# Optimization experiments

Measured on AMD Instinct MI355X. Metric: run time of the kernel, lower is better.

Reference implementation:

```python
import jax, jax.numpy as jnp
import numpy as np

B, S = 4, 4096
D_MODEL = 1024
INDEXER_DIM = 64
LOCAL_WINDOW = 16
MEDIUM_WINDOW = 64
GLOBAL_K = 32
LOCAL_SPARSE = 0.8


def _local_k_schedule(seq_len):
    # Replicates torch: k_local = max(1, int(L * (1 - local_sparse))) with Python float math
    ks = []
    for q in range(seq_len):
        L = min(q + 1, LOCAL_WINDOW)
        ks.append(max(1, int(L * (1.0 - LOCAL_SPARSE))))
    ks = np.asarray(ks, dtype=np.int32)
    return ks, int(ks.max())


def setup_inputs() -> dict:
    key = jax.random.key(0)
    kx, kl, km, kg = jax.random.split(key, 4)
    scale = D_MODEL ** -0.5
    return {
        "x": jax.random.normal(kx, (B, S, D_MODEL), jnp.float32),
        "W_local": jax.random.normal(kl, (INDEXER_DIM, D_MODEL), jnp.float32) * scale,
        "W_medium": jax.random.normal(km, (INDEXER_DIM, D_MODEL), jnp.float32) * scale,
        "W_global": jax.random.normal(kg, (INDEXER_DIM, D_MODEL), jnp.float32) * scale,
    }


def reference(x, W_local, W_medium, W_global):
    Bb, Ss, _ = x.shape
    neg_inf = jnp.array(-jnp.inf, x.dtype)
    zero = jnp.array(0.0, x.dtype)

    lf = x @ W_local.T   # [B,S,i]
    mf = x @ W_medium.T  # computed by the original but DEAD: medium branch never fires
    gf = x @ W_global.T  # [B,S,i]

    mask = jnp.full((Bb, 1, Ss, Ss), -jnp.inf, x.dtype)
    q_ix = jnp.arange(Ss)
    b_ix = jnp.arange(Bb)[:, None, None]
    qq = q_ix[None, :, None]

    # ---- local scale: causal window [max(0, q-W+1), q] ----
    offs = jnp.arange(LOCAL_WINDOW)
    win = q_ix[:, None] - (LOCAL_WINDOW - 1) + offs[None, :]  # [S,W] absolute key positions
    valid = win >= 0
    winc = jnp.clip(win, 0, Ss - 1)
    lwin = lf[:, winc]                                        # [B,S,W,i]
    lscores = jax.nn.relu(jnp.einsum('bqd,bqwd->bqw', lf, lwin))
    lscores = jnp.where(valid[None], lscores, -jnp.inf)
    ks, kmax = _local_k_schedule(Ss)
    _, tl = jax.lax.top_k(lscores, kmax)                      # [B,S,kmax] window-relative
    labs = jnp.take_along_axis(jnp.broadcast_to(winc[None], (Bb, Ss, LOCAL_WINDOW)), tl, axis=-1)
    keep = jnp.arange(kmax)[None, None, :] < jnp.asarray(ks)[None, :, None]  # [1,S,kmax]
    lvals = jnp.where(keep, zero, neg_inf)
    mask = mask.at[b_ix, 0, qq, labs].max(jnp.broadcast_to(lvals, labs.shape))

    # ---- medium scale: DEAD CODE in the original (medium_end == local_end always) ----

    # ---- global scale (active because seq_len > medium_window and global_k > 0) ----
    if Ss > MEDIUM_WINDOW and GLOBAL_K > 0:
        gs = jax.nn.relu(jnp.einsum('bqd,bkd->bqk', gf, gf))  # [B,S,S]
        j = jnp.arange(Ss)[None, :]
        banned = (j <= q_ix[:, None]) & (j >= q_ix[:, None] - (LOCAL_WINDOW - 1))  # [S,S]
        gs = jnp.where(banned[None], -jnp.inf, gs)
        _, tg = jax.lax.top_k(gs, GLOBAL_K)                   # [B,S,Kg]
        mask = mask.at[b_ix, 0, qq, tg].max(jnp.zeros(tg.shape, x.dtype))

    return mask
```

## Files before the change

kernel.cpp:

```cpp
#include <hip/hip_runtime.h>
#include <hip/hip_fp16.h>
#include <cstdint>

#define SEQ 4096
#define NB 4
#define DMODEL 1024
#define ID 64
#define LW 16
#define GK 32
#define TQ 4

#define NEG_INF (-__builtin_inff())
#define MASKED4 0xFBFFFBFFu
#define FMAT (NB * SEQ * ID)

typedef _Float16 f16x8 __attribute__((ext_vector_type(8)));
typedef float f32x4 __attribute__((ext_vector_type(4)));

__global__ __launch_bounds__(256)
void hp_feat_v11(const unsigned short* __restrict__ xu,
                 const unsigned short* __restrict__ Wlu,
                 const unsigned short* __restrict__ Wgu,
                 float* __restrict__ lf, float* __restrict__ gfT)
{
    const int tid = threadIdx.x;
    const int lane = tid & 63, w = tid >> 6;
    const long row0 = (long)blockIdx.x * 16;
    const int half = w & 1;
    const int ch = w >> 1;
    const _Float16* xp = (const _Float16*)xu;
    const _Float16* Wp = (const _Float16*)(half ? Wgu : Wlu);

    const int lr = lane & 15;
    const int kg = lane >> 4;

    const _Float16* ap = xp + (row0 + lr) * DMODEL + kg * 8;
    const _Float16* bp = Wp + (long)(ch * 32 + lr) * DMODEL + kg * 8;

    f32x4 acc0 = (f32x4){0.f, 0.f, 0.f, 0.f};
    f32x4 acc1 = (f32x4){0.f, 0.f, 0.f, 0.f};

#pragma unroll 4
    for (int k0 = 0; k0 < DMODEL; k0 += 32) {
        f16x8 av = *(const f16x8*)(ap + k0);
        f16x8 b0 = *(const f16x8*)(bp + k0);
        f16x8 b1 = *(const f16x8*)(bp + 16 * DMODEL + k0);
        acc0 = __builtin_amdgcn_mfma_f32_16x16x32_f16(av, b0, acc0, 0, 0, 0);
        acc1 = __builtin_amdgcn_mfma_f32_16x16x32_f16(av, b1, acc1, 0, 0, 0);
    }

    if (!half) {
#pragma unroll
        for (int r = 0; r < 4; r++) {
            lf[(row0 + kg * 4 + r) * ID + ch * 32 + lr]      = acc0[r];
            lf[(row0 + kg * 4 + r) * ID + ch * 32 + 16 + lr] = acc1[r];
        }
    } else {
        const int bb = (int)(row0 >> 12), s0 = (int)(row0 & 4095);
        float4 st0 = make_float4(acc0[0], acc0[1], acc0[2], acc0[3]);
        float4 st1 = make_float4(acc1[0], acc1[1], acc1[2], acc1[3]);
        *(float4*)(gfT + ((long)bb * ID + ch * 32 + lr) * SEQ + s0 + kg * 4) = st0;
        *(float4*)(gfT + ((long)bb * ID + ch * 32 + 16 + lr) * SEQ + s0 + kg * 4) = st1;
    }
}

__global__ __launch_bounds__(512, 2)
void hp_mask_v11(const float* __restrict__ lf, const float* __restrict__ gfT,
                 unsigned short* __restrict__ out)
{
    __shared__ float qv[TQ][ID];
    __shared__ float lq[TQ][ID];
    __shared__ unsigned long long red[4][8];
    __shared__ unsigned int bitmap[TQ][SEQ / 32];
    __shared__ float lsc[TQ][LW];
    __shared__ unsigned short tm[512];

    const int tid = threadIdx.x;
    const int lane = tid & 63, w = tid >> 6;
    const int bq = blockIdx.x;
    const int b = bq >> 10;
    const int q0 = (bq & 1023) * TQ;
    const float* gTb = gfT + (long)b * ID * SEQ;
    const float* lfb = lf + (long)b * SEQ * ID;

    if (tid < 256) {
        int d = tid >> 2, qi = tid & 3;
        qv[qi][d] = gTb[(long)d * SEQ + q0 + qi];
        int qi2 = tid >> 6, d2 = tid & 63;
        lq[qi2][d2] = lfb[(long)(q0 + qi2) * ID + d2];
    }
    ((unsigned int*)bitmap)[tid] = 0u;
    __syncthreads();

    float acc[2][4][TQ];
#pragma unroll
    for (int c = 0; c < 2; c++)
#pragma unroll
        for (int j = 0; j < 4; j++)
#pragma unroll
            for (int qi = 0; qi < TQ; qi++) acc[c][j][qi] = 0.f;

    const float4* gT4 = (const float4*)gTb;
#pragma unroll 1
    for (int d0 = 0; d0 < ID; d0 += 4) {
        float4 ka[4], kb[4], qd4[TQ];
#pragma unroll
        for (int dd = 0; dd < 4; dd++) {
            ka[dd] = gT4[((d0 + dd) << 10) + tid];
            kb[dd] = gT4[((d0 + dd) << 10) + 512 + tid];
        }
#pragma unroll
        for (int qi = 0; qi < TQ; qi++)
            qd4[qi] = *(const float4*)&qv[qi][d0];
#pragma unroll
        for (int dd = 0; dd < 4; dd++) {
#pragma unroll
            for (int qi = 0; qi < TQ; qi++) {
                const float qd = ((const float*)&qd4[qi])[dd];
                acc[0][0][qi] = fmaf(ka[dd].x, qd, acc[0][0][qi]);
                acc[0][1][qi] = fmaf(ka[dd].y, qd, acc[0][1][qi]);
                acc[0][2][qi] = fmaf(ka[dd].z, qd, acc[0][2][qi]);
                acc[0][3][qi] = fmaf(ka[dd].w, qd, acc[0][3][qi]);
                acc[1][0][qi] = fmaf(kb[dd].x, qd, acc[1][0][qi]);
                acc[1][1][qi] = fmaf(kb[dd].y, qd, acc[1][1][qi]);
                acc[1][2][qi] = fmaf(kb[dd].z, qd, acc[1][2][qi]);
                acc[1][3][qi] = fmaf(kb[dd].w, qd, acc[1][3][qi]);
            }
        }
    }

#pragma unroll
    for (int c = 0; c < 2; c++)
#pragma unroll
        for (int j = 0; j < 4; j++) {
            const int k = 2048 * c + 4 * tid + j;
#pragma unroll
            for (int qi = 0; qi < TQ; qi++) {
                const int q = q0 + qi;
                const bool banned = (k <= q) && (k >= q - (LW - 1));
                acc[c][j][qi] = banned ? -1.0f : fmaxf(acc[c][j][qi], 0.f);
            }
        }

    unsigned int lo[TQ], hi[TQ];
#pragma unroll
    for (int qi = 0; qi < TQ; qi++) { lo[qi] = 0u; hi[qi] = 0x7F800000u; }

#pragma unroll 1
    for (int it = 0; it < 31; ++it) {
        unsigned long long pc = 0ull;
#pragma unroll
        for (int qi = 0; qi < TQ; qi++) {
            const unsigned int mid = lo[qi] + ((hi[qi] - lo[qi]) >> 1);
            const float tf = __uint_as_float(mid - 1u);
            int cnt = 0;
#pragma unroll
            for (int c = 0; c < 2; c++)
#pragma unroll
                for (int j = 0; j < 4; j++)
                    cnt += __popcll(__ballot(acc[c][j][qi] >= tf));
            pc |= (unsigned long long)(unsigned int)cnt << (16 * qi);
        }
        if (lane == 0) red[it & 1][w] = pc;
        __syncthreads();
        unsigned long long tot = 0ull;
#pragma unroll
        for (int ww = 0; ww < 8; ww++) tot += red[it & 1][ww];
#pragma unroll
        for (int qi = 0; qi < TQ; qi++) {
            const unsigned int mid = lo[qi] + ((hi[qi] - lo[qi]) >> 1);
            const unsigned int cnt =
                (unsigned int)((tot >> (16 * qi)) & 0xFFFFull);
            if (cnt >= GK) lo[qi] = mid; else hi[qi] = mid;
        }
    }

    int T[TQ], need[TQ];
    {
        unsigned long long pg = 0ull, pe = 0ull;
#pragma unroll
        for (int qi = 0; qi < TQ; qi++) {
            const float tg = __uint_as_float(lo[qi]);
            const unsigned int eb = lo[qi] - 1u;
            int cg = 0, ce = 0;
#pragma unroll
            for (int c = 0; c < 2; c++)
#pragma unroll
                for (int j = 0; j < 4; j++) {
                    const float v = acc[c][j][qi];
                    cg += __popcll(__ballot(v >= tg));
                    ce += __popcll(__ballot(__float_as_uint(v) == eb));
                }
            pg |= (unsigned long long)(unsigned int)cg << (16 * qi);
            pe |= (unsigned long long)(unsigned int)ce << (16 * qi);
        }
        if (lane == 0) { red[2][w] = pg; red[3][w] = pe; }
        __syncthreads();
        unsigned long long tg = 0ull, te = 0ull;
#pragma unroll
        for (int ww = 0; ww < 8; ww++) { tg += red[2][ww]; te += red[3][ww]; }
#pragma unroll
        for (int qi = 0; qi < TQ; qi++) {
            const int c1 = (int)((tg >> (16 * qi)) & 0xFFFFull);
            T[qi]    = (int)((te >> (16 * qi)) & 0xFFFFull);
            need[qi] = GK - c1;
        }
    }

#pragma unroll
    for (int qi = 0; qi < TQ; qi++) {
        const bool allties = (T[qi] == need[qi]);
        const float tg = __uint_as_float(lo[qi]);
        const unsigned int eb = lo[qi] - 1u;
#pragma unroll
        for (int c = 0; c < 2; c++)
#pragma unroll
            for (int j = 0; j < 4; j++) {
                const float v = acc[c][j][qi];
                const bool sel_ = (v >= tg)
                                | (allties & (__float_as_uint(v) == eb));
                if (sel_) {
                    const int k = 2048 * c + 4 * tid + j;
                    atomicOr(&bitmap[qi][k >> 5], 1u << (k & 31));
                }
            }
    }

#pragma unroll 1
    for (int qi = 0; qi < TQ; qi++) {
        if (T[qi] > need[qi]) {
            const unsigned int eb = lo[qi] - 1u;
            unsigned int m16 = 0u;
#pragma unroll
            for (int c = 0; c < 2; c++)
#pragma unroll
                for (int j = 0; j < 4; j++)
                    if (__float_as_uint(acc[c][j][qi]) == eb)
                        m16 |= 1u << (c * 4 + j);
            tm[tid] = (unsigned short)m16;
            __syncthreads();
            if (tid == 0) {
                int taken = 0;
                for (int c = 0; c < 2 && taken < need[qi]; c++)
                    for (int t = 0; t < 512 && taken < need[qi]; t++) {
                        const unsigned int nib = ((unsigned int)tm[t] >> (c * 4)) & 15u;
                        for (int j = 0; j < 4 && taken < need[qi]; j++)
                            if ((nib >> j) & 1u) {
                                const int k = 2048 * c + 4 * t + j;
                                atomicOr(&bitmap[qi][k >> 5], 1u << (k & 31));
                                taken++;
                            }
                    }
            }
            __syncthreads();
        }
    }

    if (tid < TQ * LW) {
        int qi = tid >> 4, wnd = tid & 15;
        int q = q0 + qi;
        int win = q - (LW - 1) + wnd;
        float v = NEG_INF;
        if (win >= 0) {
            const float4* kr = (const float4*)(lfb + (long)win * ID);
            float s = 0.f;
#pragma unroll
            for (int d = 0; d < 16; d++) {
                float4 kvv = kr[d];
                const float4 qd = *(const float4*)&lq[qi][d * 4];
                s = fmaf(kvv.x, qd.x, s); s = fmaf(kvv.y, qd.y, s);
                s = fmaf(kvv.z, qd.z, s); s = fmaf(kvv.w, qd.w, s);
            }
            v = fmaxf(s, 0.f);
        }
        lsc[qi][wnd] = v;
    }
    __syncthreads();
    if (tid < TQ) {
        int qi = tid, q = q0 + qi;
        int L = (q + 1 < LW) ? q + 1 : LW;
        int ks = L / 5; if (ks < 1) ks = 1;
        for (int t = 0; t < ks; t++) {
            float best = NEG_INF; int bi = 0;
            for (int wnd = 0; wnd < LW; wnd++) {
                float v = lsc[qi][wnd];
                if (v > best) { best = v; bi = wnd; }
            }
            lsc[qi][bi] = NEG_INF;
            const int win = q - (LW - 1) + bi;
            atomicOr(&bitmap[qi][win >> 5], 1u << (win & 31));
        }
    }
    __syncthreads();

    uint4* orow = (uint4*)(out + ((long)b * SEQ + q0) * SEQ);
#pragma unroll
    for (int i = 0; i < TQ * SEQ / 8 / 512; i++) {
        const int li = i * 512 + tid;
        const int qi = li >> 9;
        const int w8 = li & 511;
        const unsigned int bits =
            (bitmap[qi][w8 >> 2] >> ((w8 & 3) * 8)) & 0xFFu;
        uint4 v;
        v.x = MASKED4 & ~(((bits &   1u) ? 0x0000FFFFu : 0u) |
                          ((bits &   2u) ? 0xFFFF0000u : 0u));
        v.y = MASKED4 & ~(((bits &   4u) ? 0x0000FFFFu : 0u) |
                          ((bits &   8u) ? 0xFFFF0000u : 0u));
        v.z = MASKED4 & ~(((bits &  16u) ? 0x0000FFFFu : 0u) |
                          ((bits &  32u) ? 0xFFFF0000u : 0u));
        v.w = MASKED4 & ~(((bits &  64u) ? 0x0000FFFFu : 0u) |
                          ((bits & 128u) ? 0xFFFF0000u : 0u));
        orow[li] = v;
    }
}

extern "C" void kernel_launch(void* const* d_in, const int* in_sizes, int n_in,
                              void* d_out, int out_size, void* d_ws, size_t ws_size,
                              hipStream_t stream) {
    const unsigned short* x  = (const unsigned short*)d_in[0];
    const unsigned short* Wl = (const unsigned short*)d_in[1];
    const unsigned short* Wg = (const unsigned short*)d_in[3];
    unsigned short* out = (unsigned short*)d_out;

    float* lf  = (float*)d_ws;
    float* gfT = lf + (long)FMAT;

    hp_feat_v11<<<NB * SEQ / 16, 256, 0, stream>>>(x, Wl, Wg, lf, gfT);
    hp_mask_v11<<<NB * SEQ / TQ, 512, 0, stream>>>(lf, gfT, out);
}
```

Measured before the change: 735.3 us.

## Process eight queries per block in mask kernel with XCD-aware block mapping

Doubles the queries handled per block from 4 to 8, so each streamed key column of gfT is reused across twice as many queries and the block count halves. The block index is remapped so each batch's blocks land on the same pair of XCDs, aiming for better L2 locality of that batch's key matrix. The binary-search counters are split across two packed reduction arrays to hold eight counts, and the dot-product loop is restructured to one dimension per step. The cost is doubled accumulator registers per thread (64 floats), which may cause spills or lower occupancy under launch_bounds(512,2), and the unshown tail of the kernel must handle TQ=8 correctly.

After: 1.280 ms. +74.0%, slower.

```diff
diff --git a/kernel.cpp b/kernel.cpp
--- a/kernel.cpp
+++ b/kernel.cpp
@@ -8,7 +8,7 @@
 #define ID 64
 #define LW 16
 #define GK 32
-#define TQ 4
+#define TQ 8
 
 #define NEG_INF (-__builtin_inff())
 #define MASKED4 0xFBFFFBFFu
@@ -65,31 +65,35 @@
 }
 
 __global__ __launch_bounds__(512, 2)
-void hp_mask_v11(const float* __restrict__ lf, const float* __restrict__ gfT,
+void hp_mask_v12(const float* __restrict__ lf, const float* __restrict__ gfT,
                  unsigned short* __restrict__ out)
 {
     __shared__ float qv[TQ][ID];
     __shared__ float lq[TQ][ID];
-    __shared__ unsigned long long red[4][8];
+    __shared__ unsigned long long redA[4][8];
+    __shared__ unsigned long long redB[4][8];
     __shared__ unsigned int bitmap[TQ][SEQ / 32];
     __shared__ float lsc[TQ][LW];
-    __shared__ unsigned short tm[512];
+    __shared__ unsigned char tm[512];
 
     const int tid = threadIdx.x;
     const int lane = tid & 63, w = tid >> 6;
-    const int bq = blockIdx.x;
-    const int b = bq >> 10;
-    const int q0 = (bq & 1023) * TQ;
+    const int bid = blockIdx.x;
+    const int xcd = bid & 7;
+    const int b = xcd >> 1;
+    const int qg = ((bid >> 3) << 1) | (xcd & 1);
+    const int q0 = qg * TQ;
     const float* gTb = gfT + (long)b * ID * SEQ;
     const float* lfb = lf + (long)b * SEQ * ID;
 
-    if (tid < 256) {
-        int d = tid >> 2, qi = tid & 3;
+    {
+        int d = tid >> 3, qi = tid & 7;
         qv[qi][d] = gTb[(long)d * SEQ + q0 + qi];
         int qi2 = tid >> 6, d2 = tid & 63;
         lq[qi2][d2] = lfb[(long)(q0 + qi2) * ID + d2];
-    }
-    ((unsigned int*)bitmap)[tid] = 0u;
+        ((unsigned int*)bitmap)[tid] = 0u;
+        ((unsigned int*)bitmap)[tid + 512] = 0u;
+    }
     __syncthreads();
 
     float acc[2][4][TQ];
@@ -101,31 +105,23 @@
             for (int qi = 0; qi < TQ; qi++) acc[c][j][qi] = 0.f;
 
     const float4* gT4 = (const float4*)gTb;
-#pragma unroll 1
-    for (int d0 = 0; d0 < ID; d0 += 4) {
-        float4 ka[4], kb[4], qd4[TQ];
-#pragma unroll
-        for (int dd = 0; dd < 4; dd++) {
-            ka[dd] = gT4[((d0 + dd) << 10) + tid];
-            kb[dd] = gT4[((d0 + dd) << 10) + 512 + tid];
-        }
-#pragma unroll
-        for (int qi = 0; qi < TQ; qi++)
-            qd4[qi] = *(const float4*)&qv[qi][d0];
-#pragma unroll
-        for (int dd = 0; dd < 4; dd++) {
-#pragma unroll
-            for (int qi = 0; qi < TQ; qi++) {
-                const float qd = ((const float*)&qd4[qi])[dd];
-                acc[0][0][qi] = fmaf(ka[dd].x, qd, acc[0][0][qi]);
-                acc[0][1][qi] = fmaf(ka[dd].y, qd, acc[0][1][qi]);
-                acc[0][2][qi] = fmaf(ka[dd].z, qd, acc[0][2][qi]);
-                acc[0][3][qi] = fmaf(ka[dd].w, qd, acc[0][3][qi]);
-                acc[1][0][qi] = fmaf(kb[dd].x, qd, acc[1][0][qi]);
-                acc[1][1][qi] = fmaf(kb[dd].y, qd, acc[1][1][qi]);
-                acc[1][2][qi] = fmaf(kb[dd].z, qd, acc[1][2][qi]);
-                acc[1][3][qi] = fmaf(kb[dd].w, qd, acc[1][3][qi]);
-            }
+#pragma unroll 2
+    for (int d = 0; d < ID; d++) {
+        const float4 ka = gT4[(d << 10) + tid];
+        const float4 kb = gT4[(d << 10) + 512 + tid];
+        float qd[TQ];
+#pragma unroll
+        for (int qi = 0; qi < TQ; qi++) qd[qi] = qv[qi][d];
+#pragma unroll
+        for (int qi = 0; qi < TQ; qi++) {
+            acc[0][0][qi] = fmaf(ka.x, qd[qi], acc[0][0][qi]);
+            acc[0][1][qi] = fmaf(ka.y, qd[qi], acc[0][1][qi]);
+            acc[0][2][qi] = fmaf(ka.z, qd[qi], acc[0][2][qi]);
+            acc[0][3][qi] = fmaf(ka.w, qd[qi], acc[0][3][qi]);
+            acc[1][0][qi] = fmaf(kb.x, qd[qi], acc[1][0][qi]);
+            acc[1][1][qi] = fmaf(kb.y, qd[qi], acc[1][1][qi]);
+            acc[1][2][qi] = fmaf(kb.z, qd[qi], acc[1][2][qi]);
+            acc[1][3][qi] = fmaf(kb.w, qd[qi], acc[1][3][qi]);
         }
     }
 
@@ -148,7 +144,7 @@
 
 #pragma unroll 1
     for (int it = 0; it < 31; ++it) {
-        unsigned long long pc = 0ull;
+        unsigned long long pcA = 0ull, pcB = 0ull;
 #pragma unroll
         for (int qi = 0; qi < TQ; qi++) {
             const unsigned int mid = lo[qi] + ((hi[qi] - lo[qi]) >> 1);
@@ -159,25 +155,29 @@
 #pragma unroll
                 for (int j = 0; j < 4; j++)
                     cnt += __popcll(__ballot(acc[c][j][qi] >= tf));
-            pc |= (unsigned long long)(unsigned int)cnt << (16 * qi);
-        }
-        if (lane == 0) red[it & 1][w] = pc;
+            if (qi < 4) pcA |= (unsigned long long)(unsigned int)cnt << (16 * qi);
+            else        pcB |= (unsigned long long)(unsigned int)cnt << (16 * (qi - 4));
+        }
+        if (lane == 0) { redA[it & 1][w] = pcA; redB[it & 1][w] = pcB; }
         __syncthreads();
-        unsigned long long tot = 0ull;
-#pragma unroll
-        for (int ww = 0; ww < 8; ww++) tot += red[it & 1][ww];
+        unsigned long long totA = 0ull, totB = 0ull;
+#pragma unroll
+        for (int ww = 0; ww < 8; ww++) {
+            totA += redA[it & 1][ww]; totB += redB[it & 1][ww];
+        }
 #pragma unroll
         for (int qi = 0; qi < TQ; qi++) {
             const unsigned int mid = lo[qi] + ((hi[qi] - lo[qi]) >> 1);
-            const unsigned int cnt =
-                (unsigned int)((tot >> (16 * qi)) & 0xFFFFull);
+            const unsigned int cnt = (qi < 4)
+                ? (unsigned int)((totA >> (16 * qi)) & 0xFFFFull)
+                : (unsigned int)((totB >> (16 * (qi - 4))) & 0xFFFFull);
             if (cnt >= GK) lo[qi] = mid; else hi[qi] = mid;
         }
     }
 
     int T[TQ], need[TQ];
     {
-        unsigned long long pg = 0ull, pe = 0ull;
+        unsigned long long pgA = 0ull, pgB = 0ull, peA = 0ull, peB = 0ull;
 #pragma unroll
         for (int qi = 0; qi < TQ; qi++) {
             const float tg = __uint_as_float(lo[qi]);
@@ -191,18 +191,33 @@
                     cg += __popcll(__ballot(v >= tg));
                     ce += __popcll(__ballot(__float_as_uint(v) == eb));
                 }
-            pg |= (unsigned long long)(unsigned int)cg << (16 * qi);
-            pe |= (unsigned long long)(unsigned int)ce << (16 * qi);
-        }
-        if (lane == 0) { red[2][w] = pg; red[3][w] = pe; }
+            if (qi < 4) {
+                pgA |= (unsigned long long)(unsigned int)cg << (16 * qi);
+                peA |= (unsigned long long)(unsigned int)ce << (16 * qi);
+            } else {
+                pgB |= (unsigned long long)(unsigned int)cg << (16 * (qi - 4));
+                peB |= (unsigned long long)(unsigned int)ce << (16 * (qi - 4));
+            }
+        }
+        if (lane == 0) {
+            redA[2][w] = pgA; redA[3][w] = peA;
+            redB[2][w] = pgB; redB[3][w] = peB;
+        }
         __syncthreads();
-        unsigned long long tg = 0ull, te = 0ull;
-#pragma unroll
-        for (int ww = 0; ww < 8; ww++) { tg += red[2][ww]; te += red[3][ww]; }
-#pragma unroll
-        for (int qi = 0; qi < TQ; qi++) {
-            const int c1 = (int)((tg >> (16 * qi)) & 0xFFFFull);
-            T[qi]    = (int)((te >> (16 * qi)) & 0xFFFFull);
+        unsigned long long tgA = 0ull, teA = 0ull, tgB = 0ull, teB = 0ull;
+#pragma unroll
+        for (int ww = 0; ww < 8; ww++) {
+            tgA += redA[2][ww]; teA += redA[3][ww];
+            tgB += redB[2][ww]; teB += redB[3][ww];
+        }
+#pragma unroll
+        for (int qi = 0; qi < TQ; qi++) {
+            const int c1 = (qi < 4)
+                ? (int)((tgA >> (16 * qi)) & 0xFFFFull)
+                : (int)((tgB >> (16 * (qi - 4))) & 0xFFFFull);
+            T[qi] = (qi < 4)
+                ? (int)((teA >> (16 * qi)) & 0xFFFFull)
+                : (int)((teB >> (16 * (qi - 4))) & 0xFFFFull);
             need[qi] = GK - c1;
         }
     }
@@ -230,14 +245,14 @@
     for (int qi = 0; qi < TQ; qi++) {
         if (T[qi] > need[qi]) {
             const unsigned int eb = lo[qi] - 1u;
-            unsigned int m16 = 0u;
+            unsigned int m8 = 0u;
 #pragma unroll
             for (int c = 0; c < 2; c++)
 #pragma unroll
                 for (int j = 0; j < 4; j++)
                     if (__float_as_uint(acc[c][j][qi]) == eb)
-                        m16 |= 1u << (c * 4 + j);
-            tm[tid] = (unsigned short)m16;
+                        m8 |= 1u << (c * 4 + j);
+            tm[tid] = (unsigned char)m8;
             __syncthreads();
             if (tid == 0) {
                 int taken = 0;
@@ -326,5 +341,5 @@
     float* gfT = lf + (long)FMAT;
 
     hp_feat_v11<<<NB * SEQ / 16, 256, 0, stream>>>(x, Wl, Wg, lf, gfT);
-    hp_mask_v11<<<NB * SEQ / TQ, 512, 0, stream>>>(lf, gfT, out);
+    hp_mask_v12<<<NB * SEQ / TQ, 512, 0, stream>>>(lf, gfT, out);
 }
```
